# Optimization experiments

Hardware: AMD Instinct MI355X
Metric: run time of the kernel (lower is better)

## Reference

```python
import jax, jax.numpy as jnp
import numpy as np

B, H, W, D = 8, 32, 32, 384      # batch, height, width, channels (=dim)
E, HID, O = 8, 1536, 384         # num_experts, mlp hidden (dim*4), out_dim
TOP_K = 2


def setup_inputs() -> dict:
    key = jax.random.key(0)
    ks = jax.random.split(key, 5)
    x = jax.random.normal(ks[0], (B, H, W, D), dtype=jnp.float32)
    # router (noise_linear unused: eval path, train=False)
    Wg = 0.02 * jax.random.normal(ks[1], (D, E), dtype=jnp.float32)
    bg = jnp.zeros((E,), dtype=jnp.float32)
    # per-expert MLP params stacked along expert axis
    W1 = 0.02 * jax.random.normal(ks[2], (E, D, HID), dtype=jnp.float32)
    b1 = jnp.zeros((E, HID), dtype=jnp.float32)
    W2 = 0.02 * jax.random.normal(ks[3], (E, HID, O), dtype=jnp.float32)
    b2 = jnp.zeros((E, O), dtype=jnp.float32)
    return {"x": x, "Wg": Wg, "bg": bg, "W1": W1, "b1": b1, "W2": W2, "b2": b2}


def reference(x, Wg, bg, W1, b1, W2, b2):
    # --- NoisyTopkRouter (eval: train=False -> no noise branch) ---
    logits = jnp.einsum('bhwd,de->bhwe', x, Wg) + bg            # [B,H,W,E]
    _, top_idx = jax.lax.top_k(logits, TOP_K)                   # [B,H,W,K]
    # mask of selected experts; sparse logits = logits where selected, -inf else
    sel = jnp.sum(jax.nn.one_hot(top_idx, E, dtype=jnp.float32), axis=-2) > 0
    sparse_logits = jnp.where(sel, logits, -jnp.inf)
    gates = jax.nn.softmax(sparse_logits, axis=-1)              # zero on non-top-k

    # --- experts: since gate is exactly 0 off the top-k, the masked
    # gather-MLP-scatter loop equals a gate-weighted sum of all expert MLPs ---
    h = jnp.einsum('bhwd,edf->bhwef', x, W1) + b1               # [B,H,W,E,HID]
    h = jax.nn.gelu(h, approximate=False)                       # torch nn.GELU = exact
    y = jnp.einsum('bhwef,efo->bhweo', h, W2) + b2              # [B,H,W,E,O]
    out = jnp.einsum('bhweo,bhwe->bhwo', y, gates)              # [B,H,W,O]
    return out
```

## Files before the change

### kernel.cpp

```cpp
#include <hip/hip_runtime.h>
#include <cmath>

#define N_TOK 8192
#define DIM   384
#define NEXP  8
#define HID   1536
#define OUTD  384
#define CAP_MT 72
#define CAP_TOK 2304
#define CAP_TB 18

typedef __attribute__((ext_vector_type(8)))  __bf16 bf16x8;
typedef __attribute__((ext_vector_type(16))) float  f32x16;
typedef __attribute__((ext_vector_type(4)))  float  f32x4;
typedef __attribute__((ext_vector_type(8)))  unsigned short u16x8;

__device__ __forceinline__ unsigned short f2bf(float f) {
    unsigned u = __float_as_uint(f);
    u += 0x7FFF + ((u >> 16) & 1);
    return (unsigned short)(u >> 16);
}

__device__ __forceinline__ float bf2f(unsigned short s) {
    return __uint_as_float(((unsigned)s) << 16);
}

__device__ __forceinline__ float gelu_fast(float x) {
    float a  = 0.70710678118654752f * x;
    float ax = fabsf(a);
    float t  = 1.0f / (1.0f + 0.3275911f * ax);
    float y  = t * (0.254829592f + t * (-0.284496736f + t * (1.421413741f
             + t * (-1.453152027f + t * 1.061405429f))));
    float er = 1.0f - y * __expf(-ax * ax);
    er = copysignf(er, a);
    return 0.5f * x * (1.0f + er);
}

__device__ __forceinline__ void cp16(const unsigned short* g, unsigned short* l) {
    __builtin_amdgcn_global_load_lds(
        (const __attribute__((address_space(1))) unsigned int*)g,
        (__attribute__((address_space(3))) unsigned int*)l, 16, 0, 0);
}

__global__ void swizzle_kernel(const float* __restrict__ W1, const float* __restrict__ W2,
                               unsigned short* __restrict__ w1s, unsigned short* __restrict__ w2s,
                               int* __restrict__ cnt) {
    if (blockIdx.x == 0 && threadIdx.x < NEXP) cnt[threadIdx.x] = 0;
    int gid = blockIdx.x * blockDim.x + threadIdx.x;
    const int T1 = NEXP * 48 * 24 * 64;
    const int T2 = NEXP * 12 * 96 * 64;
    const float* src; unsigned short* dst; int K, N, NT, KT, g;
    if (gid < T1)           { src = W1; dst = w1s; K = DIM; N = HID;  NT = 48; KT = 24; g = gid; }
    else if (gid < T1 + T2) { src = W2; dst = w2s; K = HID; N = OUTD; NT = 12; KT = 96; g = gid - T1; }
    else return;
    int l  = g & 63;
    int kt = (g >> 6) % KT;
    int nt = ((g >> 6) / KT) % NT;
    int e  = g / (64 * KT * NT);
    const float* s = src + ((size_t)e * K + kt * 16 + (l >> 5) * 8) * N + nt * 32 + (l & 31);
    unsigned short r[8];
    #pragma unroll
    for (int j = 0; j < 8; ++j) r[j] = f2bf(s[(size_t)j * N]);
    *(uint4*)(dst + (size_t)g * 8) = *(uint4*)r;
}

__global__ void router_kernel(const float* __restrict__ x, const float* __restrict__ Wg,
                              const float* __restrict__ bg, int* __restrict__ cnt,
                              int* __restrict__ btok, int* __restrict__ tokmap,
                              float* __restrict__ gmap) {
    __shared__ float WgL[NEXP * DIM];
    __shared__ int lcnt[NEXP];
    __shared__ int lbase[NEXP];
    int tid = threadIdx.x;
    for (int i = tid; i < DIM * NEXP; i += 256) {
        int ch = i >> 3, e = i & 7;
        WgL[e * DIM + ch] = Wg[i];
    }
    if (tid < NEXP) lcnt[tid] = 0;
    __syncthreads();

    int tl  = tid >> 3;
    int seg = tid & 7;
    int t   = blockIdx.x * 32 + tl;

    float lg[NEXP] = {0.f, 0.f, 0.f, 0.f, 0.f, 0.f, 0.f, 0.f};
    const float* xr = x + (size_t)t * DIM;
    #pragma unroll
    for (int d4 = 0; d4 < 12; ++d4) {
        float4 v = *(const float4*)(xr + d4 * 32 + seg * 4);
        #pragma unroll
        for (int e = 0; e < NEXP; ++e) {
            float4 w = *(const float4*)&WgL[e * DIM + d4 * 32 + seg * 4];
            lg[e] += v.x * w.x + v.y * w.y + v.z * w.z + v.w * w.w;
        }
    }
    #pragma unroll
    for (int off = 1; off < 8; off <<= 1)
        #pragma unroll
        for (int e = 0; e < NEXP; ++e)
            lg[e] += __shfl_xor(lg[e], off);

    int p0 = 0, p1 = 0, i0 = 0, i1 = 0;
    float g0 = 0.f, g1 = 0.f;
    if (seg == 0) {
        float v0 = -INFINITY, v1 = -INFINITY;
        #pragma unroll
        for (int e = 0; e < NEXP; ++e) {
            float v = lg[e] + bg[e];
            if (v > v0)      { v1 = v0; i1 = i0; v0 = v; i0 = e; }
            else if (v > v1) { v1 = v;  i1 = e; }
        }
        float e1 = expf(v1 - v0);
        g0 = 1.f / (1.f + e1);
        g1 = e1  / (1.f + e1);
        p0 = atomicAdd(&lcnt[i0], 1);
        p1 = atomicAdd(&lcnt[i1], 1);
    }
    __syncthreads();
    if (tid < NEXP) lbase[tid] = atomicAdd(&cnt[tid], lcnt[tid]);
    __syncthreads();
    if (seg == 0) {
        int o0 = lbase[i0] + p0, o1 = lbase[i1] + p1;
        btok[i0 * N_TOK + o0] = t;
        btok[i1 * N_TOK + o1] = t;
        ((int4*)tokmap)[t] = make_int4(i0, o0, i1, o1);
        ((float2*)gmap)[t] = make_float2(g0, g1);
    }
}

__global__ void gather_kernel(const float* __restrict__ x, const int* __restrict__ cnt,
                              const int* __restrict__ btok, unsigned short* __restrict__ xg) {
    int mt = blockIdx.x, e = blockIdx.y;
    int cntE = cnt[e];
    if (mt * 32 >= cntE) return;
    int tid = threadIdx.x;
    int m = tid & 31, kt0 = tid >> 5;
    int pos = mt * 32 + m;
    int idx = (pos < cntE) ? pos : cntE - 1;
    int tok = btok[e * N_TOK + idx];
    const float* xr = x + (size_t)tok * DIM;
    #pragma unroll
    for (int kk = 0; kk < 3; ++kk) {
        int kt = kt0 + kk * 8;
        #pragma unroll
        for (int kh = 0; kh < 2; ++kh) {
            float4 v0 = *(const float4*)(xr + kt * 16 + kh * 8);
            float4 v1 = *(const float4*)(xr + kt * 16 + kh * 8 + 4);
            unsigned short rr[8];
            rr[0] = f2bf(v0.x); rr[1] = f2bf(v0.y); rr[2] = f2bf(v0.z); rr[3] = f2bf(v0.w);
            rr[4] = f2bf(v1.x); rr[5] = f2bf(v1.y); rr[6] = f2bf(v1.z); rr[7] = f2bf(v1.w);
            *(uint4*)(xg + (size_t)(((e * CAP_MT + mt) * 24 + kt) * 64 + kh * 32 + m) * 8) =
                *(uint4*)rr;
        }
    }
}

__global__ __launch_bounds__(256, 3) void gemm1_kernel(
        const unsigned short* __restrict__ xg, const unsigned short* __restrict__ w1s,
        const float* __restrict__ b1, const int* __restrict__ cnt,
        unsigned short* __restrict__ h) {
    int L = blockIdx.x;
    int e = L & 7;
    int r = L >> 3;
    int nb = r % 12;
    int tb = r / 12;
    int cntE = cnt[e];
    if (tb * 128 >= cntE) return;

    __shared__ unsigned short stg[32 * 512];

    int tid = threadIdx.x;
    int wave = tid >> 6, lane = tid & 63;
    int m31 = lane & 31, kh = lane >> 5;
    int wm = wave & 1, wn = wave >> 1;

    f32x16 acc[2][2];
    #pragma unroll
    for (int i = 0; i < 2; ++i)
        #pragma unroll
        for (int j = 0; j < 2; ++j)
            acc[i][j] = (f32x16){0.f,0.f,0.f,0.f,0.f,0.f,0.f,0.f,0.f,0.f,0.f,0.f,0.f,0.f,0.f,0.f};

    const unsigned short* xa = xg  + ((size_t)(e * CAP_MT + tb * 4) * 24) * 512;
    const unsigned short* wb = w1s + ((size_t)(e * 48 + nb * 4) * 24) * 512;

    for (int ks = 0; ks < 6; ++ks) {
        __syncthreads();
        #pragma unroll
        for (int q = 0; q < 8; ++q) {
            int tl = wave * 8 + q;
            const unsigned short* src = (tl < 16)
                ? xa + ((size_t)((tl >> 2) * 24 + ks * 4 + (tl & 3))) * 512
                : wb + ((size_t)(((tl - 16) >> 2) * 24 + ks * 4 + (tl & 3))) * 512;
            cp16(src + lane * 8, &stg[tl * 512]);
        }
        __syncthreads();
        #pragma unroll
        for (int kt = 0; kt < 4; ++kt) {
            bf16x8 a0 = *(const bf16x8*)&stg[((wm * 2 + 0) * 4 + kt) * 512 + lane * 8];
            bf16x8 a1 = *(const bf16x8*)&stg[((wm * 2 + 1) * 4 + kt) * 512 + lane * 8];
            bf16x8 b0 = *(const bf16x8*)&stg[(16 + (wn * 2 + 0) * 4 + kt) * 512 + lane * 8];
            bf16x8 b1v = *(const bf16x8*)&stg[(16 + (wn * 2 + 1) * 4 + kt) * 512 + lane * 8];
            acc[0][0] = __builtin_amdgcn_mfma_f32_32x32x16_bf16(a0, b0,  acc[0][0], 0, 0, 0);
            acc[0][1] = __builtin_amdgcn_mfma_f32_32x32x16_bf16(a0, b1v, acc[0][1], 0, 0, 0);
            acc[1][0] = __builtin_amdgcn_mfma_f32_32x32x16_bf16(a1, b0,  acc[1][0], 0, 0, 0);
            acc[1][1] = __builtin_amdgcn_mfma_f32_32x32x16_bf16(a1, b1v, acc[1][1], 0, 0, 0);
        }
    }

    __syncthreads();
    char* hw = (char*)&stg[wave * 4096];
    float bv0 = b1[e * HID + nb * 128 + wn * 64 + m31];
    float bv1 = b1[e * HID + nb * 128 + wn * 64 + 32 + m31];
    #pragma unroll
    for (int im = 0; im < 2; ++im)
        #pragma unroll
        for (int in = 0; in < 2; ++in) {
            float bv = in ? bv1 : bv0;
            #pragma unroll
            for (int rr = 0; rr < 16; ++rr) {
                int row = im * 32 + (rr & 3) + 8 * (rr >> 2) + 4 * kh;
                int col = in * 32 + m31;
                unsigned boff = (unsigned)(row * 128 + col * 2) ^ ((row & 7) << 4);
                *(unsigned short*)(hw + boff) = f2bf(gelu_fast(acc[im][in][rr] + bv));
            }
        }
    #pragma unroll
    for (int mtl = 0; mtl < 2; ++mtl)
        #pragma unroll
        for (int ktl = 0; ktl < 4; ++ktl) {
            int rowl = mtl * 32 + m31;
            int coll = ktl * 16 + kh * 8;
            unsigned boff = (unsigned)(rowl * 128 + coll * 2) ^ ((rowl & 7) << 4);
            uint4 v = *(const uint4*)(hw + boff);
            int mt = tb * 4 + wm * 2 + mtl;
            int kt = nb * 8 + wn * 4 + ktl;
            *(uint4*)(h + ((size_t)((e * CAP_MT + mt) * 96 + kt)) * 512 + lane * 8) = v;
        }
}

__global__ __launch_bounds__(256, 3) void gemm2_kernel(
        const unsigned short* __restrict__ h, const unsigned short* __restrict__ w2s,
        const int* __restrict__ cnt, unsigned short* __restrict__ yp) {
    int L = blockIdx.x;
    int e = L & 7;
    int r = L >> 3;
    int nb = r % 3;
    int tb = r / 3;
    int cntE = cnt[e];
    if (tb * 128 >= cntE) return;

    __shared__ unsigned short stg[32 * 512];

    int tid = threadIdx.x;
    int wave = tid >> 6, lane = tid & 63;
    int m31 = lane & 31, kh = lane >> 5;
    int wm = wave & 1, wn = wave >> 1;

    f32x16 acc[2][2];
    #pragma unroll
    for (int i = 0; i < 2; ++i)
        #pragma unroll
        for (int j = 0; j < 2; ++j)
            acc[i][j] = (f32x16){0.f,0.f,0.f,0.f,0.f,0.f,0.f,0.f,0.f,0.f,0.f,0.f,0.f,0.f,0.f,0.f};

    const unsigned short* xa = h   + ((size_t)(e * CAP_MT + tb * 4) * 96) * 512;
    const unsigned short* wb = w2s + ((size_t)(e * 12 + nb * 4) * 96) * 512;

    for (int ks = 0; ks < 24; ++ks) {
        __syncthreads();
        #pragma unroll
        for (int q = 0; q < 8; ++q) {
            int tl = wave * 8 + q;
            const unsigned short* src = (tl < 16)
                ? xa + ((size_t)((tl >> 2) * 96 + ks * 4 + (tl & 3))) * 512
                : wb + ((size_t)(((tl - 16) >> 2) * 96 + ks * 4 + (tl & 3))) * 512;
            cp16(src + lane * 8, &stg[tl * 512]);
        }
        __syncthreads();
        #pragma unroll
        for (int kt = 0; kt < 4; ++kt) {
            bf16x8 a0 = *(const bf16x8*)&stg[((wm * 2 + 0) * 4 + kt) * 512 + lane * 8];
            bf16x8 a1 = *(const bf16x8*)&stg[((wm * 2 + 1) * 4 + kt) * 512 + lane * 8];
            bf16x8 b0 = *(const bf16x8*)&stg[(16 + (wn * 2 + 0) * 4 + kt) * 512 + lane * 8];
            bf16x8 b1v = *(const bf16x8*)&stg[(16 + (wn * 2 + 1) * 4 + kt) * 512 + lane * 8];
            acc[0][0] = __builtin_amdgcn_mfma_f32_32x32x16_bf16(a0, b0,  acc[0][0], 0, 0, 0);
            acc[0][1] = __builtin_amdgcn_mfma_f32_32x32x16_bf16(a0, b1v, acc[0][1], 0, 0, 0);
            acc[1][0] = __builtin_amdgcn_mfma_f32_32x32x16_bf16(a1, b0,  acc[1][0], 0, 0, 0);
            acc[1][1] = __builtin_amdgcn_mfma_f32_32x32x16_bf16(a1, b1v, acc[1][1], 0, 0, 0);
        }
    }

    __syncthreads();
    char* hw = (char*)&stg[wave * 4096];
    #pragma unroll
    for (int im = 0; im < 2; ++im)
        #pragma unroll
        for (int in = 0; in < 2; ++in)
            #pragma unroll
            for (int rr = 0; rr < 16; ++rr) {
                int row = im * 32 + (rr & 3) + 8 * (rr >> 2) + 4 * kh;
                int col = in * 32 + m31;
                unsigned boff = (unsigned)(row * 128 + col * 2) ^ ((row & 7) << 4);
                *(unsigned short*)(hw + boff) = f2bf(acc[im][in][rr]);
            }
    int rl8 = lane >> 3, cc = lane & 7;
    #pragma unroll
    for (int it = 0; it < 8; ++it) {
        int rowl = it * 8 + rl8;
        unsigned boff = (unsigned)(rowl * 128 + cc * 16) ^ ((rowl & 7) << 4);
        uint4 v = *(const uint4*)(hw + boff);
        int pos = tb * 128 + wm * 64 + rowl;
        *(uint4*)(yp + (size_t)(e * CAP_TOK + pos) * OUTD + nb * 128 + wn * 64 + cc * 8) = v;
    }
}

__global__ void reduce_kernel(const unsigned short* __restrict__ yp,
                              const int* __restrict__ tokmap, const float* __restrict__ gmap,
                              const float* __restrict__ b2, float* __restrict__ out) {
    int gid = blockIdx.x * 256 + threadIdx.x;
    int t = gid / 48, q = gid - t * 48;
    int4   tm = ((const int4*)tokmap)[t];
    float2 g  = ((const float2*)gmap)[t];
    const unsigned short* p0 = yp + ((size_t)(tm.x * CAP_TOK + tm.y)) * OUTD + q * 8;
    const unsigned short* p1 = yp + ((size_t)(tm.z * CAP_TOK + tm.w)) * OUTD + q * 8;
    u16x8 a = __builtin_nontemporal_load((const u16x8*)p0);
    u16x8 b = __builtin_nontemporal_load((const u16x8*)p1);
    const float* c0 = &b2[tm.x * OUTD + q * 8];
    const float* c1 = &b2[tm.z * OUTD + q * 8];
    f32x4 r0, r1;
    #pragma unroll
    for (int j = 0; j < 4; ++j) {
        r0[j] = g.x * (bf2f(a[j]) + c0[j]) + g.y * (bf2f(b[j]) + c1[j]);
        r1[j] = g.x * (bf2f(a[4 + j]) + c0[4 + j]) + g.y * (bf2f(b[4 + j]) + c1[4 + j]);
    }
    float* op = &out[(size_t)t * OUTD + q * 8];
    __builtin_nontemporal_store(r0, (f32x4*)op);
    __builtin_nontemporal_store(r1, (f32x4*)(op + 4));
}

extern "C" void kernel_launch(void* const* d_in, const int* in_sizes, int n_in,
                              void* d_out, int out_size, void* d_ws, size_t ws_size,
                              hipStream_t stream) {
    const float* x  = (const float*)d_in[0];
    const float* Wg = (const float*)d_in[1];
    const float* bg = (const float*)d_in[2];
    const float* W1 = (const float*)d_in[3];
    const float* b1 = (const float*)d_in[4];
    const float* W2 = (const float*)d_in[5];
    const float* b2 = (const float*)d_in[6];
    float* out = (float*)d_out;

    char* ws = (char*)d_ws;
    int*            cnt    = (int*)ws;
    int*            btok   = (int*)(ws + 1024);
    int*            tokmap = (int*)(ws + 263168);
    float*          gmap   = (float*)(ws + 394240);
    unsigned short* xg     = (unsigned short*)(ws + 459776);
    unsigned short* w1s    = (unsigned short*)(ws + 14615552);
    unsigned short* w2s    = (unsigned short*)(ws + 24052736);
    unsigned short* h      = (unsigned short*)(ws + 33489920);
    unsigned short* yp     = xg;

    hipLaunchKernelGGL(swizzle_kernel, dim3(4608), dim3(256), 0, stream,
                       W1, W2, w1s, w2s, cnt);
    hipLaunchKernelGGL(router_kernel, dim3(N_TOK / 32), dim3(256), 0, stream,
                       x, Wg, bg, cnt, btok, tokmap, gmap);
    hipLaunchKernelGGL(gather_kernel, dim3(CAP_MT, NEXP), dim3(256), 0, stream,
                       x, cnt, btok, xg);
    hipLaunchKernelGGL(gemm1_kernel, dim3(NEXP * 12 * CAP_TB), dim3(256), 0, stream,
                       xg, w1s, b1, cnt, h);
    hipLaunchKernelGGL(gemm2_kernel, dim3(NEXP * 3 * CAP_TB), dim3(256), 0, stream,
                       h, w2s, cnt, yp);
    hipLaunchKernelGGL(reduce_kernel, dim3(N_TOK * 48 / 256), dim3(256), 0, stream,
                       yp, tokmap, gmap, b2, out);
}
```

Measured before the change: 198.0 us.

## Double gemm2 waves per block, simplify tile-load addressing, use exact erf GELU

gemm2 moves from 4 to 8 waves per block. Each wave now computes a 64x32 output sub-tile with two MFMA accumulators instead of four, and loads four staging tiles instead of eight. The tile-load address math in both GEMMs is hoisted into a per-wave base pointer. The polynomial GELU approximation is replaced with erff-based exact GELU. More waves per block should raise latency hiding in the K loop, while erff adds some ALU cost in the gemm1 epilogue.

```diff
diff --git a/kernel.cpp b/kernel.cpp
--- a/kernel.cpp
+++ b/kernel.cpp
@@ -25,15 +25,8 @@
     return __uint_as_float(((unsigned)s) << 16);
 }
 
-__device__ __forceinline__ float gelu_fast(float x) {
-    float a  = 0.70710678118654752f * x;
-    float ax = fabsf(a);
-    float t  = 1.0f / (1.0f + 0.3275911f * ax);
-    float y  = t * (0.254829592f + t * (-0.284496736f + t * (1.421413741f
-             + t * (-1.453152027f + t * 1.061405429f))));
-    float er = 1.0f - y * __expf(-ax * ax);
-    er = copysignf(er, a);
-    return 0.5f * x * (1.0f + er);
+__device__ __forceinline__ float gelu_exact(float x) {
+    return 0.5f * x * (1.0f + erff(x * 0.70710678118654752f));
 }
 
 __device__ __forceinline__ void cp16(const unsigned short* g, unsigned short* l) {
@@ -184,16 +177,17 @@
     const unsigned short* xa = xg  + ((size_t)(e * CAP_MT + tb * 4) * 24) * 512;
     const unsigned short* wb = w1s + ((size_t)(e * 48 + nb * 4) * 24) * 512;
 
+    const unsigned short* sbase = (wave < 2)
+        ? xa + ((size_t)(wave * 2) * 24) * 512 + lane * 8
+        : wb + ((size_t)((wave - 2) * 2) * 24) * 512 + lane * 8;
+    unsigned short* dbase = &stg[wave * 8 * 512];
+
     for (int ks = 0; ks < 6; ++ks) {
         __syncthreads();
-        #pragma unroll
-        for (int q = 0; q < 8; ++q) {
-            int tl = wave * 8 + q;
-            const unsigned short* src = (tl < 16)
-                ? xa + ((size_t)((tl >> 2) * 24 + ks * 4 + (tl & 3))) * 512
-                : wb + ((size_t)(((tl - 16) >> 2) * 24 + ks * 4 + (tl & 3))) * 512;
-            cp16(src + lane * 8, &stg[tl * 512]);
-        }
+        const unsigned short* sk = sbase + ks * 2048;
+        #pragma unroll
+        for (int q = 0; q < 8; ++q)
+            cp16(sk + (q >> 2) * (24 * 512) + (q & 3) * 512, dbase + q * 512);
         __syncthreads();
         #pragma unroll
         for (int kt = 0; kt < 4; ++kt) {
@@ -222,7 +216,7 @@
                 int row = im * 32 + (rr & 3) + 8 * (rr >> 2) + 4 * kh;
                 int col = in * 32 + m31;
                 unsigned boff = (unsigned)(row * 128 + col * 2) ^ ((row & 7) << 4);
-                *(unsigned short*)(hw + boff) = f2bf(gelu_fast(acc[im][in][rr] + bv));
+                *(unsigned short*)(hw + boff) = f2bf(gelu_exact(acc[im][in][rr] + bv));
             }
         }
     #pragma unroll
@@ -239,7 +233,7 @@
         }
 }
 
-__global__ __launch_bounds__(256, 3) void gemm2_kernel(
+__global__ __launch_bounds__(512, 4) void gemm2_kernel(
         const unsigned short* __restrict__ h, const unsigned short* __restrict__ w2s,
         const int* __restrict__ cnt, unsigned short* __restrict__ yp) {
     int L = blockIdx.x;
@@ -255,63 +249,54 @@
     int tid = threadIdx.x;
     int wave = tid >> 6, lane = tid & 63;
     int m31 = lane & 31, kh = lane >> 5;
-    int wm = wave & 1, wn = wave >> 1;
-
-    f32x16 acc[2][2];
-    #pragma unroll
-    for (int i = 0; i < 2; ++i)
-        #pragma unroll
-        for (int j = 0; j < 2; ++j)
-            acc[i][j] = (f32x16){0.f,0.f,0.f,0.f,0.f,0.f,0.f,0.f,0.f,0.f,0.f,0.f,0.f,0.f,0.f,0.f};
+    int wm = wave & 1;
+    int wn = wave >> 1;
+
+    f32x16 acc[2];
+    acc[0] = (f32x16){0.f,0.f,0.f,0.f,0.f,0.f,0.f,0.f,0.f,0.f,0.f,0.f,0.f,0.f,0.f,0.f};
+    acc[1] = acc[0];
 
     const unsigned short* xa = h   + ((size_t)(e * CAP_MT + tb * 4) * 96) * 512;
     const unsigned short* wb = w2s + ((size_t)(e * 12 + nb * 4) * 96) * 512;
 
+    const unsigned short* sbase = (wave < 4)
+        ? xa + ((size_t)wave * 96) * 512 + lane * 8
+        : wb + ((size_t)(wave - 4) * 96) * 512 + lane * 8;
+    unsigned short* dbase = &stg[wave * 4 * 512];
+
     for (int ks = 0; ks < 24; ++ks) {
         __syncthreads();
-        #pragma unroll
-        for (int q = 0; q < 8; ++q) {
-            int tl = wave * 8 + q;
-            const unsigned short* src = (tl < 16)
-                ? xa + ((size_t)((tl >> 2) * 96 + ks * 4 + (tl & 3))) * 512
-                : wb + ((size_t)(((tl - 16) >> 2) * 96 + ks * 4 + (tl & 3))) * 512;
-            cp16(src + lane * 8, &stg[tl * 512]);
-        }
+        const unsigned short* sk = sbase + ks * 2048;
+        #pragma unroll
+        for (int q = 0; q < 4; ++q)
+            cp16(sk + q * 512, dbase + q * 512);
         __syncthreads();
         #pragma unroll
         for (int kt = 0; kt < 4; ++kt) {
+            bf16x8 b  = *(const bf16x8*)&stg[(16 + wn * 4 + kt) * 512 + lane * 8];
             bf16x8 a0 = *(const bf16x8*)&stg[((wm * 2 + 0) * 4 + kt) * 512 + lane * 8];
             bf16x8 a1 = *(const bf16x8*)&stg[((wm * 2 + 1) * 4 + kt) * 512 + lane * 8];
-            bf16x8 b0 = *(const bf16x8*)&stg[(16 + (wn * 2 + 0) * 4 + kt) * 512 + lane * 8];
-            bf16x8 b1v = *(const bf16x8*)&stg[(16 + (wn * 2 + 1) * 4 + kt) * 512 + lane * 8];
-            acc[0][0] = __builtin_amdgcn_mfma_f32_32x32x16_bf16(a0, b0,  acc[0][0], 0, 0, 0);
-            acc[0][1] = __builtin_amdgcn_mfma_f32_32x32x16_bf16(a0, b1v, acc[0][1], 0, 0, 0);
-            acc[1][0] = __builtin_amdgcn_mfma_f32_32x32x16_bf16(a1, b0,  acc[1][0], 0, 0, 0);
-            acc[1][1] = __builtin_amdgcn_mfma_f32_32x32x16_bf16(a1, b1v, acc[1][1], 0, 0, 0);
-        }
-    }
-
-    __syncthreads();
-    char* hw = (char*)&stg[wave * 4096];
-    #pragma unroll
-    for (int im = 0; im < 2; ++im)
-        #pragma unroll
-        for (int in = 0; in < 2; ++in)
-            #pragma unroll
-            for (int rr = 0; rr < 16; ++rr) {
-                int row = im * 32 + (rr & 3) + 8 * (rr >> 2) + 4 * kh;
-                int col = in * 32 + m31;
-                unsigned boff = (unsigned)(row * 128 + col * 2) ^ ((row & 7) << 4);
-                *(unsigned short*)(hw + boff) = f2bf(acc[im][in][rr]);
-            }
-    int rl8 = lane >> 3, cc = lane & 7;
-    #pragma unroll
-    for (int it = 0; it < 8; ++it) {
-        int rowl = it * 8 + rl8;
-        unsigned boff = (unsigned)(rowl * 128 + cc * 16) ^ ((rowl & 7) << 4);
-        uint4 v = *(const uint4*)(hw + boff);
+            acc[0] = __builtin_amdgcn_mfma_f32_32x32x16_bf16(a0, b, acc[0], 0, 0, 0);
+            acc[1] = __builtin_amdgcn_mfma_f32_32x32x16_bf16(a1, b, acc[1], 0, 0, 0);
+        }
+    }
+
+    __syncthreads();
+    char* hw = (char*)&stg[wave * 2048];
+    #pragma unroll
+    for (int s = 0; s < 2; ++s)
+        #pragma unroll
+        for (int rr = 0; rr < 16; ++rr) {
+            int rowl = s * 32 + (rr & 3) + 8 * (rr >> 2) + 4 * kh;
+            *(unsigned short*)(hw + rowl * 64 + m31 * 2) = f2bf(acc[s][rr]);
+        }
+    #pragma unroll
+    for (int it = 0; it < 4; ++it) {
+        int rowl = it * 16 + (lane >> 2);
+        int cc   = lane & 3;
+        uint4 v = *(const uint4*)(hw + rowl * 64 + cc * 16);
         int pos = tb * 128 + wm * 64 + rowl;
-        *(uint4*)(yp + (size_t)(e * CAP_TOK + pos) * OUTD + nb * 128 + wn * 64 + cc * 8) = v;
+        *(uint4*)(yp + (size_t)(e * CAP_TOK + pos) * OUTD + nb * 128 + wn * 32 + cc * 8) = v;
     }
 }
 
@@ -370,7 +355,7 @@
                        x, cnt, btok, xg);
     hipLaunchKernelGGL(gemm1_kernel, dim3(NEXP * 12 * CAP_TB), dim3(256), 0, stream,
                        xg, w1s, b1, cnt, h);
-    hipLaunchKernelGGL(gemm2_kernel, dim3(NEXP * 3 * CAP_TB), dim3(256), 0, stream,
+    hipLaunchKernelGGL(gemm2_kernel, dim3(NEXP * 3 * CAP_TB), dim3(512), 0, stream,
                        h, w2s, cnt, yp);
     hipLaunchKernelGGL(reduce_kernel, dim3(N_TOK * 48 / 256), dim3(256), 0, stream,
                        yp, tokmap, gmap, b2, out);
```

New measurement: 182.3 us. 7.9% less time.
